# Performance work log

Hardware: AMD Instinct MI355X
Metric: run time of the kernel (lower is better)

The kernel has to match this reference:

```python
import jax, jax.numpy as jnp
import numpy as np

DIM = 512      # model dim
HEADS = 8      # num heads
DH = 64        # dim_head (hard-coded in PerformerBlock)
M = 266        # nb_features = int(DH * ln(DH)) per performer_pytorch default
EPS = 1e-4     # softmax_kernel eps


def _gaussian_orthogonal_matrix(rng, m, d):
    # Faithful to performer_pytorch gaussian_orthogonal_random_matrix (scaling=0):
    # stacked QR-orthogonalized dxd blocks, rows rescaled by chi-distributed norms.
    blocks = []
    for _ in range(m // d + 1):
        q, _ = np.linalg.qr(rng.standard_normal((d, d)))
        blocks.append(q.T)
    mat = np.concatenate(blocks, 0)[:m]
    mult = np.linalg.norm(rng.standard_normal((m, d)), axis=1)
    return (mult[:, None] * mat).astype(np.float32)


def setup_inputs() -> dict:
    key = jax.random.key(0)
    ks = jax.random.split(key, 6)
    inner = HEADS * DH
    s = 0.02
    x = jax.random.normal(ks[0], (4, 4096, DIM), dtype=jnp.float32)
    Wq = jax.random.normal(ks[1], (inner, DIM), dtype=jnp.float32) * s
    Wk = jax.random.normal(ks[2], (inner, DIM), dtype=jnp.float32) * s
    Wv = jax.random.normal(ks[3], (inner, DIM), dtype=jnp.float32) * s
    Wo = jax.random.normal(ks[4], (DIM, inner), dtype=jnp.float32) * s
    bo = jnp.zeros((DIM,), dtype=jnp.float32)
    proj = jnp.asarray(_gaussian_orthogonal_matrix(np.random.default_rng(0), M, DH))
    return {"x": x, "Wq": Wq, "Wk": Wk, "Wv": Wv, "Wo": Wo, "bo": bo, "proj": proj}


def _softmax_kernel(t, proj, is_query):
    # t: (b,h,n,DH), proj: (M,DH)
    normalizer = DH ** -0.25          # 1/sqrt(sqrt(d))
    ratio = M ** -0.5
    td = jnp.einsum('bhnd,md->bhnm', t * normalizer, proj)
    diag = jnp.sum(t * t, axis=-1, keepdims=True) * 0.5 * (normalizer ** 2)
    if is_query:
        mx = jax.lax.stop_gradient(jnp.max(td, axis=-1, keepdims=True))
    else:
        mx = jax.lax.stop_gradient(jnp.max(td, axis=(-1, -2), keepdims=True))
    return ratio * (jnp.exp(td - diag - mx) + EPS)


def reference(x, Wq, Wk, Wv, Wo, bo, proj):
    b, n, _ = x.shape
    def heads(w):
        return jnp.einsum('bnd,ed->bne', x, w).reshape(b, n, HEADS, DH).transpose(0, 2, 1, 3)
    q, k, v = heads(Wq), heads(Wk), heads(Wv)  # (b,h,n,DH)
    qp = _softmax_kernel(q, proj, True)        # (b,h,n,M)
    kp = _softmax_kernel(k, proj, False)       # (b,h,n,M)
    # non-causal linear attention
    k_sum = jnp.sum(kp, axis=-2)                               # (b,h,M)
    d_inv = 1.0 / jnp.einsum('bhnm,bhm->bhn', qp, k_sum)       # (b,h,n)
    context = jnp.einsum('bhnm,bhnd->bhmd', kp, v)             # (b,h,M,DH)
    out = jnp.einsum('bhmd,bhnm,bhn->bhnd', context, qp, d_inv)
    out = out.transpose(0, 2, 1, 3).reshape(b, n, HEADS * DH)
    attn_out = out @ Wo.T + bo
    return x + attn_out
```

## Files before the change

kernel.cpp:

```cpp
#include <hip/hip_runtime.h>

#define N_ 4096
#define DIM_ 512
#define H_ 8
#define DH_ 64
#define M_ 266
#define MP_ 272
#define MP2_ 288
#define MP3_ 320
#define SLABM_ 280
#define NZ_ 8
#define NT_ 16384
#define BH_ 32

#define NORMC 0.3535533905932738f
#define RATIOC 0.06131393394849658f
#define EPSK 1e-4f
#define DIAGC 0.0625f
#define KA 0.51006971f
#define LOG2R -4.0276408f
#define LOG2E 1.4426950408889634f
#define REPS 6.131393e-6f

#define PROJP_B 0ul
#define KMAX_B  40960ul
#define KSUMA_B 41088ul
#define WO_B    82048ul
#define CTXT_B  606336ul
#define DIAGQ_B 1785984ul
#define DIAGK_B 2048128ul
#define XBF_B   2310272ul
#define WQ_B    19087488ul
#define WK_B    19611776ul
#define WV_B    20136064ul
#define CTXA_B  2310272ul
#define Q_B     20660352ul
#define K_B     37437568ul
#define VT_B    54214784ul
#define RMAXQ_B 70992000ul

typedef __bf16 bf16x8 __attribute__((ext_vector_type(8)));
typedef float f32x4 __attribute__((ext_vector_type(4)));
#define MFMA16(a, b, c) __builtin_amdgcn_mfma_f32_16x16x32_bf16((a), (b), (c), 0, 0, 0)

typedef __attribute__((address_space(1))) const unsigned int* gas_t;
typedef __attribute__((address_space(3))) unsigned int* las_t;
__device__ __forceinline__ void gload16(const void* g, void* l) {
  __builtin_amdgcn_global_load_lds((gas_t)g, (las_t)l, 16, 0, 0);
}

__device__ __forceinline__ float bfu(unsigned short u) {
  union { unsigned int i; float f; } x; x.i = ((unsigned int)u) << 16; return x.f;
}
__device__ __forceinline__ unsigned short f2bf(float f) {
  union { float f; unsigned int i; } u; u.f = f;
  unsigned int r = u.i + 0x7fffu + ((u.i >> 16) & 1u);
  return (unsigned short)(r >> 16);
}
__device__ __forceinline__ void atomicMaxF(float* addr, float val) {
  int* ai = (int*)addr;
  while (true) {
    float cur = __int_as_float(*(volatile int*)ai);
    if (val <= cur) break;
    int old = atomicCAS(ai, __float_as_int(cur), __float_as_int(val));
    if (old == __float_as_int(cur)) break;
  }
}

__global__ void prep_kernel(const float* __restrict__ x, const float* __restrict__ Wq,
                            const float* __restrict__ Wk, const float* __restrict__ Wv,
                            const float* __restrict__ Wo, const float* __restrict__ proj,
                            unsigned short* __restrict__ xbf, unsigned short* __restrict__ wqb,
                            unsigned short* __restrict__ wkb, unsigned short* __restrict__ wvb,
                            unsigned short* __restrict__ wob,
                            unsigned short* __restrict__ projp,
                            float* __restrict__ kmax, float* __restrict__ ksuma) {
  const int t0 = blockIdx.x * 256 + threadIdx.x;
  const int stride = gridDim.x * 256;
  for (int i = t0; i < 8388608 / 4; i += stride) {
    const float4 v = ((const float4*)x)[i];
    ushort4 u;
    u.x = f2bf(v.x); u.y = f2bf(v.y); u.z = f2bf(v.z); u.w = f2bf(v.w);
    ((ushort4*)xbf)[i] = u;
  }
  const float* wsrc[4] = {Wq, Wk, Wv, Wo};
  unsigned short* wdst[4] = {wqb, wkb, wvb, wob};
#pragma unroll
  for (int w = 0; w < 4; ++w) {
    for (int i = t0; i < 262144 / 4; i += stride) {
      const float4 v = ((const float4*)wsrc[w])[i];
      ushort4 u;
      u.x = f2bf(v.x); u.y = f2bf(v.y); u.z = f2bf(v.z); u.w = f2bf(v.w);
      ((ushort4*)wdst[w])[i] = u;
    }
  }
  for (int j = t0; j < MP3_ * DH_; j += stride)
    projp[j] = (j < M_ * DH_) ? f2bf(proj[j]) : (unsigned short)0;
  for (int j = t0; j < BH_; j += stride) kmax[j] = -3e38f;
  for (int j = t0; j < BH_ * MP3_; j += stride) ksuma[j] = 0.f;
}

__global__ __launch_bounds__(256) void qkv_mfma(
    const unsigned short* __restrict__ x, const unsigned short* __restrict__ Wq,
    const unsigned short* __restrict__ Wk, const unsigned short* __restrict__ Wv,
    unsigned short* __restrict__ Q, unsigned short* __restrict__ K,
    unsigned short* __restrict__ VT) {
  __shared__ unsigned short As[128 * 64];
  __shared__ unsigned short Bs[128 * 64];
  const int z = blockIdx.z;
  const unsigned short* W = (z == 0) ? Wq : (z == 1) ? Wk : Wv;
  const int t0 = blockIdx.x * 128, e0 = blockIdx.y * 128;
  const int tid = threadIdx.x;
  const int wv = tid >> 6, lane = tid & 63;
  const int r = lane & 15, q = lane >> 4;
  const int wr = (wv >> 1) * 64, wc = (wv & 1) * 64;
  f32x4 acc[4][4];
#pragma unroll
  for (int i = 0; i < 4; ++i)
#pragma unroll
    for (int j = 0; j < 4; ++j) acc[i][j] = (f32x4){0.f, 0.f, 0.f, 0.f};
  const int lrow = lane >> 3, lcol = (lane & 7) * 8;
  for (int k0 = 0; k0 < DIM_; k0 += 64) {
#pragma unroll
    for (int j = 0; j < 4; ++j) {
      const int rr = wv * 32 + j * 8;
      gload16(&x[(size_t)(t0 + rr + lrow) * DIM_ + k0 + lcol], &As[rr * 64]);
      gload16(&W[(size_t)(e0 + rr + lrow) * DIM_ + k0 + lcol], &Bs[rr * 64]);
    }
    __syncthreads();
#pragma unroll
    for (int kc = 0; kc < 2; ++kc) {
      bf16x8 af[4], bfr[4];
#pragma unroll
      for (int rt = 0; rt < 4; ++rt)
        af[rt] = *(const bf16x8*)&As[(wr + rt * 16 + r) * 64 + kc * 32 + q * 8];
#pragma unroll
      for (int ct = 0; ct < 4; ++ct)
        bfr[ct] = *(const bf16x8*)&Bs[(wc + ct * 16 + r) * 64 + kc * 32 + q * 8];
#pragma unroll
      for (int rt = 0; rt < 4; ++rt)
#pragma unroll
        for (int ct = 0; ct < 4; ++ct)
          acc[rt][ct] = MFMA16(af[rt], bfr[ct], acc[rt][ct]);
    }
    __syncthreads();
  }
  if (z < 2) {
    unsigned short* dst = (z == 0) ? Q : K;
#pragma unroll
    for (int rt = 0; rt < 4; ++rt) {
#pragma unroll
      for (int ct = 0; ct < 4; ++ct) {
        const int e = e0 + wc + ct * 16 + r;
#pragma unroll
        for (int i = 0; i < 4; ++i) {
          const int t = t0 + wr + rt * 16 + q * 4 + i;
          dst[(size_t)t * DIM_ + e] = f2bf(acc[rt][ct][i]);
        }
      }
    }
  } else {
#pragma unroll
    for (int rt = 0; rt < 4; ++rt) {
      const int t = t0 + wr + rt * 16 + q * 4;
      const int b_ = t >> 12, n = t & (N_ - 1);
#pragma unroll
      for (int ct = 0; ct < 4; ++ct) {
        const int e = e0 + wc + ct * 16 + r;
        const int h = e >> 6, dh = e & 63;
        ushort4 pk;
        pk.x = f2bf(acc[rt][ct][0]); pk.y = f2bf(acc[rt][ct][1]);
        pk.z = f2bf(acc[rt][ct][2]); pk.w = f2bf(acc[rt][ct][3]);
        *(ushort4*)&VT[((size_t)((b_ * H_ + h) * DH_ + dh)) * N_ + n] = pk;
      }
    }
  }
}

__global__ __launch_bounds__(256) void kmax_mfma(
    const unsigned short* __restrict__ K, const unsigned short* __restrict__ Qb,
    const unsigned short* __restrict__ projp,
    float* __restrict__ kmax, float* __restrict__ rmaxq,
    unsigned short* __restrict__ dq, unsigned short* __restrict__ dk) {
  __shared__ unsigned short sP[MP_][72];
  __shared__ float wm[4];
  const int bh = blockIdx.x, n0 = blockIdx.y * 256;
  const int tid = threadIdx.x;
  const int wv = tid >> 6, lane = tid & 63;
  const int r = lane & 15, q = lane >> 4;
  const int b_ = bh >> 3, h = bh & 7;
  for (int c = tid; c < MP_ * 4; c += 256) {
    const int row = c >> 2, cb = (c & 3) * 8;
    *(uint4*)&sP[row][cb] = *(const uint4*)&projp[row * DH_ + cb];
  }
  bf16x8 kb[4][2], qb[4][2];
  const int nbase = n0 + wv * 64;
#pragma unroll
  for (int st = 0; st < 4; ++st) {
    const size_t off = (size_t)(b_ * N_ + nbase + st * 16 + r) * DIM_ + h * DH_;
    kb[st][0] = *(const bf16x8*)(K + off + q * 8);
    kb[st][1] = *(const bf16x8*)(K + off + 32 + q * 8);
    qb[st][0] = *(const bf16x8*)(Qb + off + q * 8);
    qb[st][1] = *(const bf16x8*)(Qb + off + 32 + q * 8);
  }
#pragma unroll
  for (int st = 0; st < 4; ++st) {
    float sk = 0.f, sq = 0.f;
#pragma unroll
    for (int p = 0; p < 2; ++p)
#pragma unroll
      for (int e = 0; e < 8; ++e) {
        const float kv = (float)kb[st][p][e];
        const float qv = (float)qb[st][p][e];
        sk += kv * kv;
        sq += qv * qv;
      }
    sk += __shfl_xor(sk, 16, 64); sk += __shfl_xor(sk, 32, 64);
    sq += __shfl_xor(sq, 16, 64); sq += __shfl_xor(sq, 32, 64);
    if (q == 0) {
      dk[bh * N_ + nbase + st * 16 + r] = f2bf(sk * DIAGC);
      dq[bh * N_ + nbase + st * 16 + r] = f2bf(sq * DIAGC);
    }
  }
  __syncthreads();
  float km = -3e38f;
  float qm[4] = {-3e38f, -3e38f, -3e38f, -3e38f};
  for (int mt = 0; mt < 17; ++mt) {
    const bf16x8 p0 = *(const bf16x8*)&sP[mt * 16 + r][q * 8];
    const bf16x8 p1 = *(const bf16x8*)&sP[mt * 16 + r][32 + q * 8];
#pragma unroll
    for (int st = 0; st < 4; ++st) {
      f32x4 ka = (f32x4){0.f, 0.f, 0.f, 0.f};
      ka = MFMA16(p0, kb[st][0], ka);
      ka = MFMA16(p1, kb[st][1], ka);
      f32x4 qa = (f32x4){0.f, 0.f, 0.f, 0.f};
      qa = MFMA16(p0, qb[st][0], qa);
      qa = MFMA16(p1, qb[st][1], qa);
#pragma unroll
      for (int i = 0; i < 4; ++i) {
        const int m = mt * 16 + q * 4 + i;
        if (m < M_) {
          km = fmaxf(km, ka[i]);
          qm[st] = fmaxf(qm[st], qa[i]);
        }
      }
    }
  }
#pragma unroll
  for (int st = 0; st < 4; ++st) {
    float v = qm[st];
    v = fmaxf(v, __shfl_xor(v, 16, 64));
    v = fmaxf(v, __shfl_xor(v, 32, 64));
    if (q == 0) rmaxq[bh * N_ + nbase + st * 16 + r] = v;
  }
  for (int s2 = 1; s2 < 64; s2 <<= 1) km = fmaxf(km, __shfl_xor(km, s2, 64));
  if (lane == 0) wm[wv] = km;
  __syncthreads();
  if (tid == 0) {
    const float m = fmaxf(fmaxf(wm[0], wm[1]), fmaxf(wm[2], wm[3])) * NORMC;
    atomicMaxF(&kmax[bh], m);
  }
}

__global__ __launch_bounds__(256) void ctxfused_mfma(
    const unsigned short* __restrict__ K, const unsigned short* __restrict__ VT,
    const unsigned short* __restrict__ projp, const unsigned short* __restrict__ diag_k,
    const float* __restrict__ kmaxv, float* __restrict__ ksuma,
    float* __restrict__ slab) {
  __shared__ unsigned short kll[64][72];
  __shared__ unsigned short vtl[64][72];
  __shared__ unsigned short kpl[64][72];
  __shared__ float dgl[64];
  const int bh = blockIdx.x, m0 = blockIdx.y * 64, zi = blockIdx.z;
  const int nbase = zi * 512;
  const int tid = threadIdx.x;
  const int wv = tid >> 6, lane = tid & 63;
  const int r = lane & 15, q = lane >> 4;
  const int b_ = bh >> 3, h = bh & 7;
  const float km = kmaxv[bh];
  const unsigned short* prow = projp + (size_t)(m0 + wv * 16 + r) * DH_;
  const bf16x8 p0 = *(const bf16x8*)(prow + q * 8);
  const bf16x8 p1 = *(const bf16x8*)(prow + 32 + q * 8);
  const unsigned short* kbase = K + (size_t)(b_ * N_) * DIM_ + h * DH_;
  const unsigned short* vbase = VT + (size_t)bh * DH_ * N_;
  f32x4 cacc[4];
#pragma unroll
  for (int i = 0; i < 4; ++i) cacc[i] = (f32x4){0.f, 0.f, 0.f, 0.f};
  float ksa[4] = {0.f, 0.f, 0.f, 0.f};
  for (int nc = 0; nc < 8; ++nc) {
    const int n0c = nbase + nc * 64;
#pragma unroll
    for (int j = 0; j < 4; ++j) {
      const int idx = tid + j * 256;
      const int rr = idx >> 4, c4 = (idx & 15) << 2;
      *(ushort4*)&kll[rr][c4] = *(const ushort4*)&kbase[(size_t)(n0c + rr) * DIM_ + c4];
      *(ushort4*)&vtl[rr][c4] = *(const ushort4*)&vbase[(size_t)rr * N_ + n0c + c4];
    }
    if (tid < 16) {
      const ushort4 du = *(const ushort4*)&diag_k[bh * N_ + n0c + tid * 4];
      dgl[tid * 4 + 0] = bfu(du.x); dgl[tid * 4 + 1] = bfu(du.y);
      dgl[tid * 4 + 2] = bfu(du.z); dgl[tid * 4 + 3] = bfu(du.w);
    }
    __syncthreads();
#pragma unroll
    for (int nt = 0; nt < 4; ++nt) {
      const bf16x8 kb0 = *(const bf16x8*)&kll[nt * 16 + r][q * 8];
      const bf16x8 kb1 = *(const bf16x8*)&kll[nt * 16 + r][32 + q * 8];
      f32x4 acc = (f32x4){0.f, 0.f, 0.f, 0.f};
      acc = MFMA16(p0, kb0, acc);
      acc = MFMA16(p1, kb1, acc);
      const float dgk = dgl[nt * 16 + r];
#pragma unroll
      for (int i = 0; i < 4; ++i) {
        const int m = m0 + wv * 16 + q * 4 + i;
        float kp = 0.f;
        if (m < M_) {
          const float arg = fminf(NORMC * acc[i] - dgk - km, 0.f);
          kp = RATIOC * (__expf(arg) + EPSK);
        }
        kpl[wv * 16 + q * 4 + i][nt * 16 + r] = f2bf(kp);
        ksa[i] += kp;
      }
    }
    __syncthreads();
    {
      const bf16x8 a0 = *(const bf16x8*)&kpl[wv * 16 + r][q * 8];
      const bf16x8 a1 = *(const bf16x8*)&kpl[wv * 16 + r][32 + q * 8];
#pragma unroll
      for (int ct = 0; ct < 4; ++ct) {
        const bf16x8 b0 = *(const bf16x8*)&vtl[ct * 16 + r][q * 8];
        const bf16x8 b1 = *(const bf16x8*)&vtl[ct * 16 + r][32 + q * 8];
        cacc[ct] = MFMA16(a0, b0, cacc[ct]);
        cacc[ct] = MFMA16(a1, b1, cacc[ct]);
      }
    }
    __syncthreads();
  }
#pragma unroll
  for (int i = 0; i < 4; ++i)
    for (int s2 = 1; s2 < 16; s2 <<= 1) ksa[i] += __shfl_xor(ksa[i], s2, 64);
  if (r == 0) {
#pragma unroll
    for (int i = 0; i < 4; ++i)
      atomicAdd(&ksuma[bh * MP3_ + m0 + wv * 16 + q * 4 + i], ksa[i]);
  }
  float* sl = slab + (size_t)(bh * NZ_ + zi) * SLABM_ * DH_;
#pragma unroll
  for (int ct = 0; ct < 4; ++ct) {
#pragma unroll
    for (int i = 0; i < 4; ++i) {
      const int m = m0 + wv * 16 + q * 4 + i;
      if (m < SLABM_) sl[(size_t)m * DH_ + ct * 16 + r] = cacc[ct][i];
    }
  }
}

__global__ __launch_bounds__(256) void pack_kernel(const float* __restrict__ slab,
                                                   unsigned short* __restrict__ ctxT) {
  __shared__ float t[64][65];
  const int bh = blockIdx.x, m0 = blockIdx.y * 64;
  const int tid = threadIdx.x;
  const int mr = tid >> 4, d4 = (tid & 15) * 4;
#pragma unroll
  for (int pass = 0; pass < 4; ++pass) {
    const int ml = pass * 16 + mr;
    const int m = m0 + ml;
    float4 s = {0.f, 0.f, 0.f, 0.f};
    if (m < SLABM_) {
#pragma unroll
      for (int z = 0; z < NZ_; ++z) {
        const float4 v =
            *(const float4*)&slab[((size_t)(bh * NZ_ + z) * SLABM_ + m) * DH_ + d4];
        s.x += v.x; s.y += v.y; s.z += v.z; s.w += v.w;
      }
    }
    t[ml][d4 + 0] = s.x; t[ml][d4 + 1] = s.y; t[ml][d4 + 2] = s.z; t[ml][d4 + 3] = s.w;
  }
  __syncthreads();
  const int mc = tid & 63, dbase = tid >> 6;
  const int mo = m0 + mc;
  if (mo < MP2_) {
#pragma unroll
    for (int j = 0; j < 16; ++j) {
      const int d = dbase + j * 4;
      ctxT[((size_t)bh * DH_ + d) * MP2_ + mo] = f2bf(t[mc][d]);
    }
  }
}

__global__ __launch_bounds__(256) void qpout_mfma(
    const unsigned short* __restrict__ Qb, const unsigned short* __restrict__ projp,
    const float* __restrict__ rmaxq,
    const unsigned short* __restrict__ diag_q, const float* __restrict__ ksuma,
    const unsigned short* __restrict__ ctxT, unsigned short* __restrict__ attn) {
  __shared__ union SM {
    unsigned short sP[MP_][72];
    unsigned int qps[4][16][149];
  } sm;
  const int bh = blockIdx.x, n0 = blockIdx.y * 64;
  const int tid = threadIdx.x;
  const int wv = tid >> 6, lane = tid & 63;
  const int r = lane & 15, q = lane >> 4;
  const int b_ = bh >> 3, h = bh & 7;
  for (int c = tid; c < MP_ * 4; c += 256) {
    const int row = c >> 2, cb = (c & 3) * 8;
    *(uint4*)&sm.sP[row][cb] = *(const uint4*)&projp[row * DH_ + cb];
  }
  bf16x8 qb0, qb1;
  {
    const unsigned short* qrow = Qb + (size_t)(b_ * N_ + n0 + wv * 16 + r) * DIM_ + h * DH_;
    qb0 = *(const bf16x8*)(qrow + q * 8);
    qb1 = *(const bf16x8*)(qrow + 32 + q * 8);
  }
  const float rm = rmaxq[bh * N_ + n0 + wv * 16 + r];
  const float dg = bfu(diag_q[bh * N_ + n0 + wv * 16 + r]);
  const float Cl = LOG2R - dg * LOG2E - rm * KA;
  __syncthreads();
  unsigned int pk0[17], pk1[17];
  float part = 0.f;
#pragma unroll
  for (int mt = 0; mt < 17; ++mt) {
    const bf16x8 p0 = *(const bf16x8*)&sm.sP[mt * 16 + r][q * 8];
    const bf16x8 p1 = *(const bf16x8*)&sm.sP[mt * 16 + r][32 + q * 8];
    f32x4 acc = (f32x4){0.f, 0.f, 0.f, 0.f};
    acc = MFMA16(p0, qb0, acc);
    acc = MFMA16(p1, qb1, acc);
    const f32x4 kl = *(const f32x4*)&ksuma[bh * MP3_ + mt * 16 + q * 4];
    {
      const float s0 = fminf(acc[0] * KA + Cl, LOG2R);
      const float s1 = fminf(acc[1] * KA + Cl, LOG2R);
      const float e0 = exp2f(s0) + REPS;
      const float e1 = exp2f(s1) + REPS;
      unsigned int pkk;
      asm("v_cvt_pk_bf16_f32 %0, %1, %2" : "=v"(pkk) : "v"(e0), "v"(e1));
      pk0[mt] = pkk;
      union { unsigned int u; float f; } lo, hi;
      lo.u = pkk << 16; hi.u = pkk & 0xffff0000u;
      part += lo.f * kl[0] + hi.f * kl[1];
    }
    {
      const float s0 = fminf(acc[2] * KA + Cl, LOG2R);
      const float s1 = fminf(acc[3] * KA + Cl, LOG2R);
      const float e0 = exp2f(s0) + REPS;
      const float e1 = exp2f(s1) + REPS;
      unsigned int pkk;
      asm("v_cvt_pk_bf16_f32 %0, %1, %2" : "=v"(pkk) : "v"(e0), "v"(e1));
      pk1[mt] = pkk;
      union { unsigned int u; float f; } lo, hi;
      lo.u = pkk << 16; hi.u = pkk & 0xffff0000u;
      part += lo.f * kl[2] + hi.f * kl[3];
    }
  }
  __syncthreads();
#pragma unroll
  for (int mt = 0; mt < 17; ++mt)
    *(uint2*)&sm.qps[wv][r][mt * 8 + q * 2] = make_uint2(pk0[mt], pk1[mt]);
  *(uint2*)&sm.qps[wv][r][136 + q * 2] = make_uint2(0u, 0u);
  part += __shfl_xor(part, 16, 64);
  part += __shfl_xor(part, 32, 64);
  const float dinv = 1.f / fmaxf(part, 1e-30f);
  f32x4 oacc[4];
#pragma unroll
  for (int i = 0; i < 4; ++i) oacc[i] = (f32x4){0.f, 0.f, 0.f, 0.f};
  const unsigned short* cbase = ctxT + (size_t)bh * DH_ * MP2_;
#pragma unroll
  for (int kc = 0; kc < 9; ++kc) {
    const bf16x8 af = *(const bf16x8*)&sm.qps[wv][r][kc * 16 + q * 4];
#pragma unroll
    for (int dt = 0; dt < 4; ++dt) {
      const bf16x8 bfr = *(const bf16x8*)&cbase[(size_t)(dt * 16 + r) * MP2_ + kc * 32 + q * 8];
      oacc[dt] = MFMA16(af, bfr, oacc[dt]);
    }
  }
  float dv[4];
#pragma unroll
  for (int i = 0; i < 4; ++i)
    dv[i] = __shfl(dinv, (lane & 48) | (q * 4 + i), 64);
#pragma unroll
  for (int dt = 0; dt < 4; ++dt) {
    const int d = dt * 16 + r;
#pragma unroll
    for (int i = 0; i < 4; ++i) {
      const int nn = wv * 16 + q * 4 + i;
      attn[(size_t)(b_ * N_ + n0 + nn) * DIM_ + h * DH_ + d] = f2bf(oacc[dt][i] * dv[i]);
    }
  }
}

__global__ __launch_bounds__(256) void final_mfma(
    const unsigned short* __restrict__ attn, const unsigned short* __restrict__ Wo,
    const float* __restrict__ bo, const float* __restrict__ x,
    float* __restrict__ out) {
  __shared__ unsigned short As[128 * 64];
  __shared__ unsigned short Bs[128 * 64];
  const int t0 = blockIdx.x * 128, e0 = blockIdx.y * 128;
  const int tid = threadIdx.x;
  const int wv = tid >> 6, lane = tid & 63;
  const int r = lane & 15, q = lane >> 4;
  const int wr = (wv >> 1) * 64, wc = (wv & 1) * 64;
  f32x4 acc[4][4];
#pragma unroll
  for (int i = 0; i < 4; ++i)
#pragma unroll
    for (int j = 0; j < 4; ++j) acc[i][j] = (f32x4){0.f, 0.f, 0.f, 0.f};
  const int lrow = lane >> 3, lcol = (lane & 7) * 8;
  for (int k0 = 0; k0 < DIM_; k0 += 64) {
#pragma unroll
    for (int j = 0; j < 4; ++j) {
      const int rr = wv * 32 + j * 8;
      gload16(&attn[(size_t)(t0 + rr + lrow) * DIM_ + k0 + lcol], &As[rr * 64]);
      gload16(&Wo[(size_t)(e0 + rr + lrow) * DIM_ + k0 + lcol], &Bs[rr * 64]);
    }
    __syncthreads();
#pragma unroll
    for (int kc = 0; kc < 2; ++kc) {
      bf16x8 af[4], bfr[4];
#pragma unroll
      for (int rt = 0; rt < 4; ++rt)
        af[rt] = *(const bf16x8*)&As[(wr + rt * 16 + r) * 64 + kc * 32 + q * 8];
#pragma unroll
      for (int ct = 0; ct < 4; ++ct)
        bfr[ct] = *(const bf16x8*)&Bs[(wc + ct * 16 + r) * 64 + kc * 32 + q * 8];
#pragma unroll
      for (int rt = 0; rt < 4; ++rt)
#pragma unroll
        for (int ct = 0; ct < 4; ++ct)
          acc[rt][ct] = MFMA16(af[rt], bfr[ct], acc[rt][ct]);
    }
    __syncthreads();
  }
#pragma unroll
  for (int rt = 0; rt < 4; ++rt) {
#pragma unroll
    for (int ct = 0; ct < 4; ++ct) {
      const int c = e0 + wc + ct * 16 + r;
      const float bov = bo[c];
#pragma unroll
      for (int i = 0; i < 4; ++i) {
        const int t = t0 + wr + rt * 16 + q * 4 + i;
        out[(size_t)t * DIM_ + c] = acc[rt][ct][i] + bov + x[(size_t)t * DIM_ + c];
      }
    }
  }
}

extern "C" void kernel_launch(void* const* d_in, const int* in_sizes, int n_in,
                              void* d_out, int out_size, void* d_ws, size_t ws_size,
                              hipStream_t stream) {
  const float* x = (const float*)d_in[0];
  const float* Wq = (const float*)d_in[1];
  const float* Wk = (const float*)d_in[2];
  const float* Wv = (const float*)d_in[3];
  const float* Wo = (const float*)d_in[4];
  const float* bo = (const float*)d_in[5];
  const float* proj = (const float*)d_in[6];
  char* ws = (char*)d_ws;
  unsigned short* projp = (unsigned short*)(ws + PROJP_B);
  float* kmax = (float*)(ws + KMAX_B);
  float* ksuma = (float*)(ws + KSUMA_B);
  float* ctxa = (float*)(ws + CTXA_B);
  unsigned short* ctxT = (unsigned short*)(ws + CTXT_B);
  unsigned short* diag_q = (unsigned short*)(ws + DIAGQ_B);
  unsigned short* diag_k = (unsigned short*)(ws + DIAGK_B);
  unsigned short* xbf = (unsigned short*)(ws + XBF_B);
  unsigned short* wqb = (unsigned short*)(ws + WQ_B);
  unsigned short* wkb = (unsigned short*)(ws + WK_B);
  unsigned short* wvb = (unsigned short*)(ws + WV_B);
  unsigned short* wob = (unsigned short*)(ws + WO_B);
  unsigned short* Q = (unsigned short*)(ws + Q_B);
  unsigned short* K = (unsigned short*)(ws + K_B);
  unsigned short* VT = (unsigned short*)(ws + VT_B);
  float* rmaxq = (float*)(ws + RMAXQ_B);
  unsigned short* attn = K;
  float* out = (float*)d_out;

  prep_kernel<<<1024, 256, 0, stream>>>(x, Wq, Wk, Wv, Wo, proj,
                                        xbf, wqb, wkb, wvb, wob, projp, kmax, ksuma);
  qkv_mfma<<<dim3(NT_ / 128, DIM_ / 128, 3), 256, 0, stream>>>(xbf, wqb, wkb, wvb, Q, K, VT);
  kmax_mfma<<<dim3(BH_, N_ / 256), 256, 0, stream>>>(K, Q, projp, kmax, rmaxq, diag_q, diag_k);
  ctxfused_mfma<<<dim3(BH_, 5, NZ_), 256, 0, stream>>>(K, VT, projp, diag_k, kmax, ksuma, ctxa);
  pack_kernel<<<dim3(BH_, 5), 256, 0, stream>>>(ctxa, ctxT);
  qpout_mfma<<<dim3(BH_, 64), 256, 0, stream>>>(Q, projp, rmaxq, diag_q, ksuma, ctxT, attn);
  final_mfma<<<dim3(NT_ / 128, DIM_ / 128), 256, 0, stream>>>(attn, wob, bo, x, out);
}
```

Baseline: 269.8 us.

## Double-buffer LDS tiles in QKV and output GEMMs, drop redundant barrier

The QKV projection and final output GEMMs now use two 32-wide K slices of shared memory. The next slice's global-to-LDS load is issued while MFMAs run on the current one, so each K step needs one barrier instead of two. A __syncthreads in the context kernel is also removed, because each wave only reads back the kp rows it wrote itself. The intent is to hide global load latency and cut barrier stalls, at the cost of relying on the load-completion semantics of gload16 for correctness.

```diff
diff --git a/kernel.cpp b/kernel.cpp
--- a/kernel.cpp
+++ b/kernel.cpp
@@ -105,8 +105,8 @@
     const unsigned short* __restrict__ Wk, const unsigned short* __restrict__ Wv,
     unsigned short* __restrict__ Q, unsigned short* __restrict__ K,
     unsigned short* __restrict__ VT) {
-  __shared__ unsigned short As[128 * 64];
-  __shared__ unsigned short Bs[128 * 64];
+  __shared__ unsigned short As[2][128 * 32];
+  __shared__ unsigned short Bs[2][128 * 32];
   const int z = blockIdx.z;
   const unsigned short* W = (z == 0) ? Wq : (z == 1) ? Wk : Wv;
   const int t0 = blockIdx.x * 128, e0 = blockIdx.y * 128;
@@ -119,32 +119,35 @@
   for (int i = 0; i < 4; ++i)
 #pragma unroll
     for (int j = 0; j < 4; ++j) acc[i][j] = (f32x4){0.f, 0.f, 0.f, 0.f};
-  const int lrow = lane >> 3, lcol = (lane & 7) * 8;
-  for (int k0 = 0; k0 < DIM_; k0 += 64) {
-#pragma unroll
-    for (int j = 0; j < 4; ++j) {
-      const int rr = wv * 32 + j * 8;
-      gload16(&x[(size_t)(t0 + rr + lrow) * DIM_ + k0 + lcol], &As[rr * 64]);
-      gload16(&W[(size_t)(e0 + rr + lrow) * DIM_ + k0 + lcol], &Bs[rr * 64]);
-    }
+  const int lrow2 = lane >> 2, lcol2 = (lane & 3) * 8;
+#define QKV_STAGE(buf, k0)                                                               \
+  {                                                                                      \
+    _Pragma("unroll") for (int j = 0; j < 2; ++j) {                                      \
+      const int rb = wv * 32 + j * 16;                                                   \
+      gload16(&x[(size_t)(t0 + rb + lrow2) * DIM_ + (k0) + lcol2], &As[buf][rb * 32]);   \
+      gload16(&W[(size_t)(e0 + rb + lrow2) * DIM_ + (k0) + lcol2], &Bs[buf][rb * 32]);   \
+    }                                                                                    \
+  }
+#define QKV_COMPUTE(buf)                                                                 \
+  {                                                                                      \
+    bf16x8 af[4], bfr[4];                                                                \
+    _Pragma("unroll") for (int rt = 0; rt < 4; ++rt)                                     \
+      af[rt] = *(const bf16x8*)&As[buf][(wr + rt * 16 + r) * 32 + q * 8];                \
+    _Pragma("unroll") for (int ct = 0; ct < 4; ++ct)                                     \
+      bfr[ct] = *(const bf16x8*)&Bs[buf][(wc + ct * 16 + r) * 32 + q * 8];               \
+    _Pragma("unroll") for (int rt = 0; rt < 4; ++rt)                                     \
+      _Pragma("unroll") for (int ct = 0; ct < 4; ++ct)                                   \
+        acc[rt][ct] = MFMA16(af[rt], bfr[ct], acc[rt][ct]);                              \
+  }
+  QKV_STAGE(0, 0);
+  __syncthreads();
+#pragma unroll
+  for (int it = 1; it < 16; ++it) {
+    QKV_STAGE(it & 1, it * 32);
+    QKV_COMPUTE((it - 1) & 1);
     __syncthreads();
-#pragma unroll
-    for (int kc = 0; kc < 2; ++kc) {
-      bf16x8 af[4], bfr[4];
-#pragma unroll
-      for (int rt = 0; rt < 4; ++rt)
-        af[rt] = *(const bf16x8*)&As[(wr + rt * 16 + r) * 64 + kc * 32 + q * 8];
-#pragma unroll
-      for (int ct = 0; ct < 4; ++ct)
-        bfr[ct] = *(const bf16x8*)&Bs[(wc + ct * 16 + r) * 64 + kc * 32 + q * 8];
-#pragma unroll
-      for (int rt = 0; rt < 4; ++rt)
-#pragma unroll
-        for (int ct = 0; ct < 4; ++ct)
-          acc[rt][ct] = MFMA16(af[rt], bfr[ct], acc[rt][ct]);
-    }
-    __syncthreads();
-  }
+  }
+  QKV_COMPUTE(1);
   if (z < 2) {
     unsigned short* dst = (z == 0) ? Q : K;
 #pragma unroll
@@ -322,7 +325,6 @@
         ksa[i] += kp;
       }
     }
-    __syncthreads();
     {
       const bf16x8 a0 = *(const bf16x8*)&kpl[wv * 16 + r][q * 8];
       const bf16x8 a1 = *(const bf16x8*)&kpl[wv * 16 + r][32 + q * 8];
@@ -491,8 +493,8 @@
     const unsigned short* __restrict__ attn, const unsigned short* __restrict__ Wo,
     const float* __restrict__ bo, const float* __restrict__ x,
     float* __restrict__ out) {
-  __shared__ unsigned short As[128 * 64];
-  __shared__ unsigned short Bs[128 * 64];
+  __shared__ unsigned short As[2][128 * 32];
+  __shared__ unsigned short Bs[2][128 * 32];
   const int t0 = blockIdx.x * 128, e0 = blockIdx.y * 128;
   const int tid = threadIdx.x;
   const int wv = tid >> 6, lane = tid & 63;
@@ -503,32 +505,35 @@
   for (int i = 0; i < 4; ++i)
 #pragma unroll
     for (int j = 0; j < 4; ++j) acc[i][j] = (f32x4){0.f, 0.f, 0.f, 0.f};
-  const int lrow = lane >> 3, lcol = (lane & 7) * 8;
-  for (int k0 = 0; k0 < DIM_; k0 += 64) {
-#pragma unroll
-    for (int j = 0; j < 4; ++j) {
-      const int rr = wv * 32 + j * 8;
-      gload16(&attn[(size_t)(t0 + rr + lrow) * DIM_ + k0 + lcol], &As[rr * 64]);
-      gload16(&Wo[(size_t)(e0 + rr + lrow) * DIM_ + k0 + lcol], &Bs[rr * 64]);
-    }
+  const int lrow2 = lane >> 2, lcol2 = (lane & 3) * 8;
+#define FIN_STAGE(buf, k0)                                                                 \
+  {                                                                                        \
+    _Pragma("unroll") for (int j = 0; j < 2; ++j) {                                        \
+      const int rb = wv * 32 + j * 16;                                                     \
+      gload16(&attn[(size_t)(t0 + rb + lrow2) * DIM_ + (k0) + lcol2], &As[buf][rb * 32]);  \
+      gload16(&Wo[(size_t)(e0 + rb + lrow2) * DIM_ + (k0) + lcol2], &Bs[buf][rb * 32]);    \
+    }                                                                                      \
+  }
+#define FIN_COMPUTE(buf)                                                                   \
+  {                                                                                        \
+    bf16x8 af[4], bfr[4];                                                                  \
+    _Pragma("unroll") for (int rt = 0; rt < 4; ++rt)                                       \
+      af[rt] = *(const bf16x8*)&As[buf][(wr + rt * 16 + r) * 32 + q * 8];                  \
+    _Pragma("unroll") for (int ct = 0; ct < 4; ++ct)                                       \
+      bfr[ct] = *(const bf16x8*)&Bs[buf][(wc + ct * 16 + r) * 32 + q * 8];                 \
+    _Pragma("unroll") for (int rt = 0; rt < 4; ++rt)                                       \
+      _Pragma("unroll") for (int ct = 0; ct < 4; ++ct)                                     \
+        acc[rt][ct] = MFMA16(af[rt], bfr[ct], acc[rt][ct]);                                \
+  }
+  FIN_STAGE(0, 0);
+  __syncthreads();
+#pragma unroll
+  for (int it = 1; it < 16; ++it) {
+    FIN_STAGE(it & 1, it * 32);
+    FIN_COMPUTE((it - 1) & 1);
     __syncthreads();
-#pragma unroll
-    for (int kc = 0; kc < 2; ++kc) {
-      bf16x8 af[4], bfr[4];
-#pragma unroll
-      for (int rt = 0; rt < 4; ++rt)
-        af[rt] = *(const bf16x8*)&As[(wr + rt * 16 + r) * 64 + kc * 32 + q * 8];
-#pragma unroll
-      for (int ct = 0; ct < 4; ++ct)
-        bfr[ct] = *(const bf16x8*)&Bs[(wc + ct * 16 + r) * 64 + kc * 32 + q * 8];
-#pragma unroll
-      for (int rt = 0; rt < 4; ++rt)
-#pragma unroll
-        for (int ct = 0; ct < 4; ++ct)
-          acc[rt][ct] = MFMA16(af[rt], bfr[ct], acc[rt][ct]);
-    }
-    __syncthreads();
-  }
+  }
+  FIN_COMPUTE(1);
 #pragma unroll
   for (int rt = 0; rt < 4; ++rt) {
 #pragma unroll
```

Result: slower. 300.7 us (+11.4%).
